# Performance work log

Measured on AMD Instinct MI355X. Metric: run time of the kernel, lower is better.

Reference implementation:

```python
import jax, jax.numpy as jnp
import numpy as np

B, L, D, E, H = 4, 2048, 512, 8, 1024

def setup_inputs() -> dict:
    key = jax.random.key(0)
    k1, k2, k3, k4 = jax.random.split(key, 4)
    x = jax.random.normal(k1, (B, L, D), dtype=jnp.float32)
    weights = jax.random.uniform(k2, (B, L, E), dtype=jnp.float32)
    w1 = jax.random.normal(k3, (E, D, H), dtype=jnp.float32) * 0.02
    b1 = jnp.zeros((E, H), dtype=jnp.float32)
    w2 = jax.random.normal(k4, (E, H, D), dtype=jnp.float32) * 0.02
    b2 = jnp.zeros((E, D), dtype=jnp.float32)
    return {"x": x, "weights": weights, "w1": w1, "b1": b1, "w2": w2, "b2": b2}

def reference(x, weights, w1, b1, w2, b2):
    # h: [B, L, E, H]
    h = jnp.einsum('bld,edh->bleh', x, w1) + b1[None, None, :, :]
    h = jax.nn.gelu(h, approximate=False)  # torch F.gelu default is exact (erf)
    # out: [B, L, E, D]
    out = jnp.einsum('bleh,ehd->bled', h, w2) + b2[None, None, :, :]
    # weighted sum over experts -> [B, L, D]
    return jnp.einsum('bled,ble->bld', out, weights)
```

## Files before the change

### kernel.cpp

```cpp
#include <hip/hip_runtime.h>
#include <hip/hip_bf16.h>

#define DEV __device__ __forceinline__

typedef __bf16 bf16;
typedef __bf16 bf16x4 __attribute__((ext_vector_type(4)));
typedef __bf16 bf16x8 __attribute__((ext_vector_type(8)));
typedef float f32x4 __attribute__((ext_vector_type(4)));

static constexpr int Bb = 4, Ll = 2048, Dd = 512, Ee = 8, Hh = 1024;
static constexpr int Mm = Bb * Ll;
static constexpr int GKS = Ee * Hh;

DEV void gload_lds16(const void* g, void* l) {
  __builtin_amdgcn_global_load_lds(
      (const __attribute__((address_space(1))) unsigned int*)g,
      (__attribute__((address_space(3))) unsigned int*)l, 16, 0, 0);
}

DEV float gelu_fast(float h) {
  const float k = 0.7978845608028654f * 2.0f * 1.4426950408889634f;
  float h2 = h * h;
  float y = h * (k + (0.044715f * k) * h2);
  float t = exp2f(y);
  return h - h * __frcp_rn(t + 1.0f);
}

__global__ void cvt_x_kernel(const float* __restrict__ in, bf16* __restrict__ out, int n4) {
  int i = blockIdx.x * blockDim.x + threadIdx.x;
  if (i < n4) {
    float4 v = ((const float4*)in)[i];
    bf16x4 o = {(bf16)v.x, (bf16)v.y, (bf16)v.z, (bf16)v.w};
    ((bf16x4*)out)[i] = o;
  }
}

__global__ void transpose_cvt(const float* __restrict__ in, bf16* __restrict__ out,
                              int R, int C, size_t in_es, size_t out_es, int out_rs) {
  __shared__ float tile[64][65];
  const int e = blockIdx.z;
  const float* ip = in + (size_t)e * in_es;
  bf16* op = out + (size_t)e * out_es;
  const int r0 = blockIdx.y * 64, c0 = blockIdx.x * 64;
  const int tc = threadIdx.x & 63, tr = threadIdx.x >> 6;
#pragma unroll
  for (int i = 0; i < 16; ++i) {
    const int r = tr + i * 4;
    tile[r][tc] = ip[(size_t)(r0 + r) * C + c0 + tc];
  }
  __syncthreads();
  const int wr = threadIdx.x & 63, wc0 = threadIdx.x >> 6;
#pragma unroll
  for (int i = 0; i < 16; ++i) {
    const int c = wc0 + i * 4;
    op[(size_t)(c0 + c) * out_rs + r0 + wr] = (bf16)tile[wr][c];
  }
}

template <int ARS, int BRS>
DEV void gemm_core(const bf16* __restrict__ Ag, const bf16* __restrict__ Bg,
                   int ksteps, f32x4 (&acc)[4][4], bf16* As, bf16* Bs) {
  const int t = threadIdx.x;
  const int lane = t & 63;
  const int w = t >> 6;
  const int srow = t >> 3;
  const int sseg = t & 7;
  const int wr = w >> 1, wc = w & 1;
  const int fr = lane & 15;
  const int fg = lane >> 4;

  for (int s = 0; s < ksteps; ++s) {
    __syncthreads();
#pragma unroll
    for (int i = 0; i < 4; ++i) {
      const int row = i * 32 + srow;
      const int q = sseg ^ (row & 7);
      gload_lds16(Ag + (size_t)row * ARS + s * 64 + q * 8,
                  (char*)As + i * 4096 + w * 1024);
      gload_lds16(Bg + (size_t)row * BRS + s * 64 + q * 8,
                  (char*)Bs + i * 4096 + w * 1024);
    }
    __syncthreads();
#pragma unroll
    for (int kk = 0; kk < 2; ++kk) {
      bf16x8 af[4], bfr[4];
#pragma unroll
      for (int mi = 0; mi < 4; ++mi) {
        const int row = wr * 64 + mi * 16 + fr;
        const int q = (kk * 4 + fg) ^ (row & 7);
        af[mi] = *(const bf16x8*)((const char*)As + row * 128 + q * 16);
      }
#pragma unroll
      for (int ni = 0; ni < 4; ++ni) {
        const int row = wc * 64 + ni * 16 + fr;
        const int q = (kk * 4 + fg) ^ (row & 7);
        bfr[ni] = *(const bf16x8*)((const char*)Bs + row * 128 + q * 16);
      }
#pragma unroll
      for (int mi = 0; mi < 4; ++mi)
#pragma unroll
        for (int ni = 0; ni < 4; ++ni)
          acc[mi][ni] = __builtin_amdgcn_mfma_f32_16x16x32_bf16(
              af[mi], bfr[ni], acc[mi][ni], 0, 0, 0);
    }
  }
}

DEV void gemm_core_r(const bf16* __restrict__ Ag, size_t a_rs,
                     const bf16* __restrict__ Bg, size_t b_rs,
                     int ksteps, f32x4 (&acc)[4][4], bf16* As, bf16* Bs) {
  const int t = threadIdx.x;
  const int lane = t & 63;
  const int w = t >> 6;
  const int srow = t >> 3;
  const int sseg = t & 7;
  const int wr = w >> 1, wc = w & 1;
  const int fr = lane & 15;
  const int fg = lane >> 4;
  for (int s = 0; s < ksteps; ++s) {
    __syncthreads();
#pragma unroll
    for (int i = 0; i < 4; ++i) {
      const int row = i * 32 + srow;
      const int q = sseg ^ (row & 7);
      gload_lds16(Ag + (size_t)row * a_rs + s * 64 + q * 8,
                  (char*)As + i * 4096 + w * 1024);
      gload_lds16(Bg + (size_t)row * b_rs + s * 64 + q * 8,
                  (char*)Bs + i * 4096 + w * 1024);
    }
    __syncthreads();
#pragma unroll
    for (int kk = 0; kk < 2; ++kk) {
      bf16x8 af[4], bfr[4];
#pragma unroll
      for (int mi = 0; mi < 4; ++mi) {
        const int row = wr * 64 + mi * 16 + fr;
        const int q = (kk * 4 + fg) ^ (row & 7);
        af[mi] = *(const bf16x8*)((const char*)As + row * 128 + q * 16);
      }
#pragma unroll
      for (int ni = 0; ni < 4; ++ni) {
        const int row = wc * 64 + ni * 16 + fr;
        const int q = (kk * 4 + fg) ^ (row & 7);
        bfr[ni] = *(const bf16x8*)((const char*)Bs + row * 128 + q * 16);
      }
#pragma unroll
      for (int mi = 0; mi < 4; ++mi)
#pragma unroll
        for (int ni = 0; ni < 4; ++ni)
          acc[mi][ni] = __builtin_amdgcn_mfma_f32_16x16x32_bf16(
              af[mi], bfr[ni], acc[mi][ni], 0, 0, 0);
    }
  }
}

__global__ __launch_bounds__(256) void ffn_stage1_t(
    const bf16* __restrict__ xb, const bf16* __restrict__ w1t,
    const float* __restrict__ b1, const float* __restrict__ wts,
    bf16* __restrict__ G) {
  __shared__ __align__(16) bf16 As[128 * 64];
  __shared__ __align__(16) bf16 Bs[128 * 64];
  __shared__ float b1s[128];
  __shared__ float wls[128];
  const int mt = blockIdx.x, ht = blockIdx.y, e = blockIdx.z;
  const int t = threadIdx.x;
  if (t < 128) b1s[t] = b1[e * Hh + ht * 128 + t];
  else wls[t - 128] = wts[((size_t)mt * 128 + (t - 128)) * Ee + e];

  f32x4 acc[4][4] = {};
  const bf16* Ag = xb + (size_t)mt * 128 * Dd;
  const bf16* Bg = w1t + ((size_t)e * Hh + (size_t)ht * 128) * Dd;
  gemm_core<Dd, Dd>(Ag, Bg, Dd / 64, acc, As, Bs);

  const int lane = t & 63, w = t >> 6;
  const int wr = w >> 1, wc = w & 1, fr = lane & 15, fq = lane >> 4;
  float bcol[4];
#pragma unroll
  for (int ni = 0; ni < 4; ++ni) bcol[ni] = b1s[wc * 64 + ni * 16 + fr];
  bf16* gp = G + ((size_t)mt * 128 + wr * 64 + fq * 4) * GKS
               + (size_t)e * Hh + ht * 128 + wc * 64 + fr;
#pragma unroll
  for (int mi = 0; mi < 4; ++mi) {
#pragma unroll
    for (int r = 0; r < 4; ++r) {
      const float wgt = wls[wr * 64 + mi * 16 + fq * 4 + r];
#pragma unroll
      for (int ni = 0; ni < 4; ++ni) {
        float v = acc[mi][ni][r] + bcol[ni];
        gp[(size_t)(mi * 16 + r) * GKS + ni * 16] = (bf16)(gelu_fast(v) * wgt);
      }
    }
  }
}

__global__ __launch_bounds__(256) void ffn_stage2_partial(
    const bf16* __restrict__ G, const bf16* __restrict__ w2t,
    float* __restrict__ P, int kchunk) {
  __shared__ __align__(16) bf16 As[128 * 64];
  __shared__ __align__(16) bf16 Bs[128 * 64];
  const int mt = blockIdx.x, nt = blockIdx.y, s = blockIdx.z;
  f32x4 acc[4][4] = {};
  const bf16* Ag = G + (size_t)mt * 128 * GKS + (size_t)s * kchunk;
  const bf16* Bg = w2t + (size_t)nt * 128 * GKS + (size_t)s * kchunk;
  gemm_core<GKS, GKS>(Ag, Bg, kchunk / 64, acc, As, Bs);

  float* Pp = P + (size_t)s * Mm * Dd;
  const int t = threadIdx.x;
  const int lane = t & 63, w = t >> 6;
  const int wr = w >> 1, wc = w & 1, fr = lane & 15, fq = lane >> 4;
#pragma unroll
  for (int mi = 0; mi < 4; ++mi)
#pragma unroll
    for (int r = 0; r < 4; ++r) {
      const size_t m = (size_t)mt * 128 + wr * 64 + mi * 16 + fq * 4 + r;
#pragma unroll
      for (int ni = 0; ni < 4; ++ni) {
        const int d = nt * 128 + wc * 64 + ni * 16 + fr;
        Pp[m * Dd + d] = acc[mi][ni][r];
      }
    }
}

__global__ __launch_bounds__(256) void reduce_bias(
    const float* __restrict__ P, const float* __restrict__ wts,
    const float* __restrict__ b2, float* __restrict__ out, int S) {
  const int n4 = Mm * Dd / 4;
  int i = blockIdx.x * 256 + threadIdx.x;
  if (i >= n4) return;
  const int m = i / (Dd / 4);
  const int d0 = (i % (Dd / 4)) * 4;
  float4 a = ((const float4*)P)[i];
  for (int s = 1; s < S; ++s) {
    float4 p = ((const float4*)P)[(size_t)s * n4 + i];
    a.x += p.x; a.y += p.y; a.z += p.z; a.w += p.w;
  }
  const float* wr = wts + (size_t)m * Ee;
#pragma unroll
  for (int e = 0; e < Ee; ++e) {
    const float w = wr[e];
    float4 b = *(const float4*)(b2 + e * Dd + d0);
    a.x += w * b.x; a.y += w * b.y; a.z += w * b.z; a.w += w * b.w;
  }
  ((float4*)out)[i] = a;
}

__global__ __launch_bounds__(256) void ffn_stage1(
    const bf16* __restrict__ xb, const bf16* __restrict__ w1t,
    const float* __restrict__ b1, const float* __restrict__ wts,
    bf16* __restrict__ G, int e0, int gks) {
  __shared__ __align__(16) bf16 As[128 * 64];
  __shared__ __align__(16) bf16 Bs[128 * 64];
  const int mt = blockIdx.x, ht = blockIdx.y, le = blockIdx.z;
  const int e = e0 + le;
  f32x4 acc[4][4] = {};
  const bf16* Ag = xb + (size_t)mt * 128 * Dd;
  const bf16* Bg = w1t + ((size_t)e * Hh + (size_t)ht * 128) * Dd;
  gemm_core_r(Ag, Dd, Bg, Dd, Dd / 64, acc, As, Bs);
  const int t = threadIdx.x;
  const int lane = t & 63, w = t >> 6;
  const int wr = w >> 1, wc = w & 1, fr = lane & 15, fq = lane >> 4;
#pragma unroll
  for (int mi = 0; mi < 4; ++mi)
#pragma unroll
    for (int r = 0; r < 4; ++r) {
      const int m = mt * 128 + wr * 64 + mi * 16 + fq * 4 + r;
      const float wgt = wts[(size_t)m * Ee + e];
#pragma unroll
      for (int ni = 0; ni < 4; ++ni) {
        const int h = ht * 128 + wc * 64 + ni * 16 + fr;
        float v = acc[mi][ni][r] + b1[e * Hh + h];
        G[(size_t)m * gks + (size_t)le * Hh + h] = (bf16)(gelu_fast(v) * wgt);
      }
    }
}

__global__ __launch_bounds__(256) void ffn_stage2(
    const bf16* __restrict__ G, const bf16* __restrict__ w2t,
    const float* __restrict__ b2, const float* __restrict__ wts,
    float* __restrict__ out, int e0, int gks, int first) {
  __shared__ __align__(16) bf16 As[128 * 64];
  __shared__ __align__(16) bf16 Bs[128 * 64];
  __shared__ float b2s[Ee][128];
  __shared__ float wls[128][Ee];
  const int mt = blockIdx.x, nt = blockIdx.y;
  const int t = threadIdx.x;
  if (first) {
    for (int i = t; i < Ee * 128; i += 256) {
      const int ee = i >> 7, d = i & 127;
      b2s[ee][d] = b2[ee * Dd + nt * 128 + d];
    }
    for (int i = t; i < 128 * Ee; i += 256) {
      const int r = i >> 3, ee = i & 7;
      wls[r][ee] = wts[((size_t)mt * 128 + r) * Ee + ee];
    }
  }
  f32x4 acc[4][4] = {};
  const bf16* Ag = G + (size_t)mt * 128 * gks;
  const bf16* Bg = w2t + (size_t)nt * 128 * ((size_t)Ee * Hh) + (size_t)e0 * Hh;
  gemm_core_r(Ag, gks, Bg, (size_t)Ee * Hh, gks / 64, acc, As, Bs);
  const int lane = t & 63, w = t >> 6;
  const int wr = w >> 1, wc = w & 1, fr = lane & 15, fq = lane >> 4;
#pragma unroll
  for (int mi = 0; mi < 4; ++mi)
#pragma unroll
    for (int r = 0; r < 4; ++r) {
      const int lrow = wr * 64 + mi * 16 + fq * 4 + r;
      const size_t m = (size_t)mt * 128 + lrow;
#pragma unroll
      for (int ni = 0; ni < 4; ++ni) {
        const int lcol = wc * 64 + ni * 16 + fr;
        const size_t oidx = m * Dd + nt * 128 + lcol;
        float v = acc[mi][ni][r];
        if (first) {
          float bias = 0.f;
#pragma unroll
          for (int ee = 0; ee < Ee; ++ee) bias += wls[lrow][ee] * b2s[ee][lcol];
          out[oidx] = v + bias;
        } else {
          out[oidx] += v;
        }
      }
    }
}

extern "C" void kernel_launch(void* const* d_in, const int* in_sizes, int n_in,
                              void* d_out, int out_size, void* d_ws, size_t ws_size,
                              hipStream_t stream) {
  const float* x   = (const float*)d_in[0];
  const float* wts = (const float*)d_in[1];
  const float* w1  = (const float*)d_in[2];
  const float* b1  = (const float*)d_in[3];
  const float* w2  = (const float*)d_in[4];
  const float* b2  = (const float*)d_in[5];
  float* out = (float*)d_out;

  char* ws = (char*)d_ws;
  size_t off = 0;
  bf16* xb  = (bf16*)(ws + off); off += (size_t)Mm * Dd * 2;
  bf16* w1t = (bf16*)(ws + off); off += (size_t)Ee * Hh * Dd * 2;
  bf16* w2t = (bf16*)(ws + off); off += (size_t)Dd * Ee * Hh * 2;

  const size_t gfull = (size_t)Mm * Ee * Hh * 2;
  const size_t psz   = (size_t)Mm * Dd * 4;

  cvt_x_kernel<<<(Mm * Dd / 4 + 255) / 256, 256, 0, stream>>>(x, xb, Mm * Dd / 4);
  transpose_cvt<<<dim3(Hh / 64, Dd / 64, Ee), 256, 0, stream>>>(
      w1, w1t, Dd, Hh, (size_t)Dd * Hh, (size_t)Hh * Dd, Dd);
  transpose_cvt<<<dim3(Dd / 64, Hh / 64, Ee), 256, 0, stream>>>(
      w2, w2t, Hh, Dd, (size_t)Hh * Dd, (size_t)Hh, Ee * Hh);

  int S = 0;
  if (ws_size >= off + gfull + 4 * psz) S = 4;
  else if (ws_size >= off + gfull + 2 * psz) S = 2;

  if (S >= 2) {
    bf16* G = (bf16*)(ws + off);
    float* P = (float*)(ws + off + gfull);
    ffn_stage1_t<<<dim3(Mm / 128, Hh / 128, Ee), 256, 0, stream>>>(
        xb, w1t, b1, wts, G);
    ffn_stage2_partial<<<dim3(Mm / 128, Dd / 128, S), 256, 0, stream>>>(
        G, w2t, P, GKS / S);
    reduce_bias<<<(Mm * Dd / 4 + 255) / 256, 256, 0, stream>>>(P, wts, b2, out, S);
  } else {
    bf16* G = (bf16*)(ws + off);
    size_t avail = ws_size > off ? ws_size - off : 0;
    size_t slab = (size_t)Mm * Hh * 2;
    int Ec = (int)(avail / slab);
    if (Ec < 1) Ec = 1;
    if (Ec > Ee) Ec = Ee;
    int first = 1;
    for (int e0 = 0; e0 < Ee;) {
      const int ec = (Ee - e0 < Ec) ? (Ee - e0) : Ec;
      const int gks = ec * Hh;
      ffn_stage1<<<dim3(Mm / 128, Hh / 128, ec), 256, 0, stream>>>(
          xb, w1t, b1, wts, G, e0, gks);
      ffn_stage2<<<dim3(Mm / 128, Dd / 128), 256, 0, stream>>>(
          G, w2t, b2, wts, out, e0, gks, first);
      e0 += ec;
      first = 0;
    }
  }
}
```

Measured before the change: 240.0 us.

## Use 256x256 double-buffered MFMA tiles for both FFN GEMM stages

Adds a 512-thread GEMM core that computes 256x256 output tiles. It double-buffers the global-to-LDS loads behind vmcnt waits and raises wave priority around the MFMA bursts. Both stage kernels switch to this core and store their epilogues as vector writes (bf16x4 / f32x4), using a transposed accumulator layout. The larger tiles are meant to improve operand reuse and hide load latency. The cost is 128KB of LDS per block, which limits occupancy, and the low-workspace expert-chunked fallback path is removed.

```diff
diff --git a/kernel.cpp b/kernel.cpp
--- a/kernel.cpp
+++ b/kernel.cpp
@@ -58,167 +58,146 @@
 }
 
 template <int ARS, int BRS>
-DEV void gemm_core(const bf16* __restrict__ Ag, const bf16* __restrict__ Bg,
-                   int ksteps, f32x4 (&acc)[4][4], bf16* As, bf16* Bs) {
+DEV void gemm256_core(const bf16* __restrict__ Ag, const bf16* __restrict__ Bg,
+                      int nt, f32x4 (&acc)[8][4], char* lds) {
   const int t = threadIdx.x;
   const int lane = t & 63;
-  const int w = t >> 6;
+  const int wid = t >> 6;
+  const int wm = wid >> 2, wn = wid & 3;
+  const int fr = lane & 15, fg = lane >> 4;
   const int srow = t >> 3;
   const int sseg = t & 7;
-  const int wr = w >> 1, wc = w & 1;
-  const int fr = lane & 15;
-  const int fg = lane >> 4;
-
-  for (int s = 0; s < ksteps; ++s) {
-    __syncthreads();
+
+  auto stage = [&](int kt, int p) {
+    char* As = lds + p * 65536;
+    char* Bs = lds + p * 65536 + 32768;
 #pragma unroll
     for (int i = 0; i < 4; ++i) {
-      const int row = i * 32 + srow;
+      const int row = i * 64 + srow;
       const int q = sseg ^ (row & 7);
-      gload_lds16(Ag + (size_t)row * ARS + s * 64 + q * 8,
-                  (char*)As + i * 4096 + w * 1024);
-      gload_lds16(Bg + (size_t)row * BRS + s * 64 + q * 8,
-                  (char*)Bs + i * 4096 + w * 1024);
-    }
-    __syncthreads();
-#pragma unroll
-    for (int kk = 0; kk < 2; ++kk) {
-      bf16x8 af[4], bfr[4];
-#pragma unroll
-      for (int mi = 0; mi < 4; ++mi) {
-        const int row = wr * 64 + mi * 16 + fr;
-        const int q = (kk * 4 + fg) ^ (row & 7);
-        af[mi] = *(const bf16x8*)((const char*)As + row * 128 + q * 16);
-      }
-#pragma unroll
-      for (int ni = 0; ni < 4; ++ni) {
-        const int row = wc * 64 + ni * 16 + fr;
-        const int q = (kk * 4 + fg) ^ (row & 7);
-        bfr[ni] = *(const bf16x8*)((const char*)Bs + row * 128 + q * 16);
-      }
-#pragma unroll
-      for (int mi = 0; mi < 4; ++mi)
-#pragma unroll
-        for (int ni = 0; ni < 4; ++ni)
-          acc[mi][ni] = __builtin_amdgcn_mfma_f32_16x16x32_bf16(
-              af[mi], bfr[ni], acc[mi][ni], 0, 0, 0);
-    }
-  }
-}
-
-DEV void gemm_core_r(const bf16* __restrict__ Ag, size_t a_rs,
-                     const bf16* __restrict__ Bg, size_t b_rs,
-                     int ksteps, f32x4 (&acc)[4][4], bf16* As, bf16* Bs) {
-  const int t = threadIdx.x;
-  const int lane = t & 63;
-  const int w = t >> 6;
-  const int srow = t >> 3;
-  const int sseg = t & 7;
-  const int wr = w >> 1, wc = w & 1;
-  const int fr = lane & 15;
-  const int fg = lane >> 4;
-  for (int s = 0; s < ksteps; ++s) {
-    __syncthreads();
-#pragma unroll
-    for (int i = 0; i < 4; ++i) {
-      const int row = i * 32 + srow;
-      const int q = sseg ^ (row & 7);
-      gload_lds16(Ag + (size_t)row * a_rs + s * 64 + q * 8,
-                  (char*)As + i * 4096 + w * 1024);
-      gload_lds16(Bg + (size_t)row * b_rs + s * 64 + q * 8,
-                  (char*)Bs + i * 4096 + w * 1024);
-    }
-    __syncthreads();
-#pragma unroll
-    for (int kk = 0; kk < 2; ++kk) {
-      bf16x8 af[4], bfr[4];
-#pragma unroll
-      for (int mi = 0; mi < 4; ++mi) {
-        const int row = wr * 64 + mi * 16 + fr;
-        const int q = (kk * 4 + fg) ^ (row & 7);
-        af[mi] = *(const bf16x8*)((const char*)As + row * 128 + q * 16);
-      }
-#pragma unroll
-      for (int ni = 0; ni < 4; ++ni) {
-        const int row = wc * 64 + ni * 16 + fr;
-        const int q = (kk * 4 + fg) ^ (row & 7);
-        bfr[ni] = *(const bf16x8*)((const char*)Bs + row * 128 + q * 16);
-      }
-#pragma unroll
-      for (int mi = 0; mi < 4; ++mi)
-#pragma unroll
-        for (int ni = 0; ni < 4; ++ni)
-          acc[mi][ni] = __builtin_amdgcn_mfma_f32_16x16x32_bf16(
-              af[mi], bfr[ni], acc[mi][ni], 0, 0, 0);
-    }
-  }
-}
-
-__global__ __launch_bounds__(256) void ffn_stage1_t(
+      gload_lds16(Ag + (size_t)row * ARS + kt * 64 + q * 8, As + i * 8192 + wid * 1024);
+      gload_lds16(Bg + (size_t)row * BRS + kt * 64 + q * 8, Bs + i * 8192 + wid * 1024);
+    }
+  };
+
+  stage(0, 0);
+  for (int kt = 0; kt < nt; ++kt) {
+    const int p = kt & 1;
+    if (kt + 1 < nt) {
+      stage(kt + 1, p ^ 1);
+      asm volatile("s_waitcnt vmcnt(8)" ::: "memory");
+    } else {
+      asm volatile("s_waitcnt vmcnt(0)" ::: "memory");
+    }
+    __builtin_amdgcn_s_barrier();
+    const char* As = lds + p * 65536;
+    const char* Bs = lds + p * 65536 + 32768;
+    bf16x8 bfrag[4][2];
+#pragma unroll
+    for (int q = 0; q < 4; ++q) {
+      if (q == 0) {
+#pragma unroll
+        for (int fj = 0; fj < 4; ++fj)
+#pragma unroll
+          for (int kk = 0; kk < 2; ++kk) {
+            const int row = wn * 64 + fj * 16 + fr;
+            const int seg = (kk * 4 + fg) ^ (row & 7);
+            bfrag[fj][kk] = *(const bf16x8*)(Bs + row * 128 + seg * 16);
+          }
+      }
+      bf16x8 af[2][2];
+#pragma unroll
+      for (int fil = 0; fil < 2; ++fil)
+#pragma unroll
+        for (int kk = 0; kk < 2; ++kk) {
+          const int row = wm * 128 + (q * 2 + fil) * 16 + fr;
+          const int seg = (kk * 4 + fg) ^ (row & 7);
+          af[fil][kk] = *(const bf16x8*)(As + row * 128 + seg * 16);
+        }
+      __builtin_amdgcn_s_barrier();
+      asm volatile("s_waitcnt lgkmcnt(0)" ::: "memory");
+      __builtin_amdgcn_sched_barrier(0);
+      __builtin_amdgcn_s_setprio(1);
+#pragma unroll
+      for (int fil = 0; fil < 2; ++fil)
+#pragma unroll
+        for (int fj = 0; fj < 4; ++fj)
+#pragma unroll
+          for (int kk = 0; kk < 2; ++kk)
+            acc[q * 2 + fil][fj] = __builtin_amdgcn_mfma_f32_16x16x32_bf16(
+                bfrag[fj][kk], af[fil][kk], acc[q * 2 + fil][fj], 0, 0, 0);
+      __builtin_amdgcn_s_setprio(0);
+      __builtin_amdgcn_s_barrier();
+    }
+  }
+}
+
+__global__ __launch_bounds__(512, 2) void ffn_stage1_256(
     const bf16* __restrict__ xb, const bf16* __restrict__ w1t,
     const float* __restrict__ b1, const float* __restrict__ wts,
     bf16* __restrict__ G) {
-  __shared__ __align__(16) bf16 As[128 * 64];
-  __shared__ __align__(16) bf16 Bs[128 * 64];
-  __shared__ float b1s[128];
-  __shared__ float wls[128];
-  const int mt = blockIdx.x, ht = blockIdx.y, e = blockIdx.z;
-  const int t = threadIdx.x;
-  if (t < 128) b1s[t] = b1[e * Hh + ht * 128 + t];
-  else wls[t - 128] = wts[((size_t)mt * 128 + (t - 128)) * Ee + e];
-
-  f32x4 acc[4][4] = {};
-  const bf16* Ag = xb + (size_t)mt * 128 * Dd;
-  const bf16* Bg = w1t + ((size_t)e * Hh + (size_t)ht * 128) * Dd;
-  gemm_core<Dd, Dd>(Ag, Bg, Dd / 64, acc, As, Bs);
-
-  const int lane = t & 63, w = t >> 6;
-  const int wr = w >> 1, wc = w & 1, fr = lane & 15, fq = lane >> 4;
-  float bcol[4];
-#pragma unroll
-  for (int ni = 0; ni < 4; ++ni) bcol[ni] = b1s[wc * 64 + ni * 16 + fr];
-  bf16* gp = G + ((size_t)mt * 128 + wr * 64 + fq * 4) * GKS
-               + (size_t)e * Hh + ht * 128 + wc * 64 + fr;
-#pragma unroll
-  for (int mi = 0; mi < 4; ++mi) {
-#pragma unroll
-    for (int r = 0; r < 4; ++r) {
-      const float wgt = wls[wr * 64 + mi * 16 + fq * 4 + r];
-#pragma unroll
-      for (int ni = 0; ni < 4; ++ni) {
-        float v = acc[mi][ni][r] + bcol[ni];
-        gp[(size_t)(mi * 16 + r) * GKS + ni * 16] = (bf16)(gelu_fast(v) * wgt);
-      }
-    }
-  }
-}
-
-__global__ __launch_bounds__(256) void ffn_stage2_partial(
+  __shared__ __align__(16) char lds[131072];
+  __shared__ float b1s[256];
+  __shared__ float wls[256];
+  const int mt = blockIdx.x;
+  const int e = blockIdx.y >> 2, ht2 = blockIdx.y & 3;
+  const int t = threadIdx.x;
+  if (t < 256) b1s[t] = b1[e * Hh + ht2 * 256 + t];
+  else wls[t - 256] = wts[((size_t)mt * 256 + (t - 256)) * Ee + e];
+
+  f32x4 acc[8][4] = {};
+  const bf16* Ag = xb + (size_t)mt * 256 * Dd;
+  const bf16* Bg = w1t + ((size_t)e * Hh + (size_t)ht2 * 256) * Dd;
+  gemm256_core<Dd, Dd>(Ag, Bg, Dd / 64, acc, lds);
+
+  const int lane = t & 63, wid = t >> 6;
+  const int wm = wid >> 2, wn = wid & 3;
+  const int fr = lane & 15, fq = lane >> 4;
+  float b1v[4][4];
+#pragma unroll
+  for (int fj = 0; fj < 4; ++fj)
+#pragma unroll
+    for (int r = 0; r < 4; ++r) b1v[fj][r] = b1s[wn * 64 + fj * 16 + fq * 4 + r];
+#pragma unroll
+  for (int fi = 0; fi < 8; ++fi) {
+    const int m = mt * 256 + wm * 128 + fi * 16 + fr;
+    const float wgt = wls[wm * 128 + fi * 16 + fr];
+    bf16* gp = G + (size_t)m * GKS + e * Hh + ht2 * 256 + wn * 64 + fq * 4;
+#pragma unroll
+    for (int fj = 0; fj < 4; ++fj) {
+      bf16x4 o;
+#pragma unroll
+      for (int r = 0; r < 4; ++r) {
+        float v = acc[fi][fj][r] + b1v[fj][r];
+        o[r] = (bf16)(gelu_fast(v) * wgt);
+      }
+      *(bf16x4*)(gp + fj * 16) = o;
+    }
+  }
+}
+
+__global__ __launch_bounds__(512, 2) void ffn_stage2_256(
     const bf16* __restrict__ G, const bf16* __restrict__ w2t,
     float* __restrict__ P, int kchunk) {
-  __shared__ __align__(16) bf16 As[128 * 64];
-  __shared__ __align__(16) bf16 Bs[128 * 64];
+  __shared__ __align__(16) char lds[131072];
   const int mt = blockIdx.x, nt = blockIdx.y, s = blockIdx.z;
-  f32x4 acc[4][4] = {};
-  const bf16* Ag = G + (size_t)mt * 128 * GKS + (size_t)s * kchunk;
-  const bf16* Bg = w2t + (size_t)nt * 128 * GKS + (size_t)s * kchunk;
-  gemm_core<GKS, GKS>(Ag, Bg, kchunk / 64, acc, As, Bs);
+  f32x4 acc[8][4] = {};
+  const bf16* Ag = G + (size_t)mt * 256 * GKS + (size_t)s * kchunk;
+  const bf16* Bg = w2t + (size_t)nt * 256 * GKS + (size_t)s * kchunk;
+  gemm256_core<GKS, GKS>(Ag, Bg, kchunk / 64, acc, lds);
 
   float* Pp = P + (size_t)s * Mm * Dd;
   const int t = threadIdx.x;
-  const int lane = t & 63, w = t >> 6;
-  const int wr = w >> 1, wc = w & 1, fr = lane & 15, fq = lane >> 4;
-#pragma unroll
-  for (int mi = 0; mi < 4; ++mi)
-#pragma unroll
-    for (int r = 0; r < 4; ++r) {
-      const size_t m = (size_t)mt * 128 + wr * 64 + mi * 16 + fq * 4 + r;
-#pragma unroll
-      for (int ni = 0; ni < 4; ++ni) {
-        const int d = nt * 128 + wc * 64 + ni * 16 + fr;
-        Pp[m * Dd + d] = acc[mi][ni][r];
-      }
-    }
+  const int lane = t & 63, wid = t >> 6;
+  const int wm = wid >> 2, wn = wid & 3;
+  const int fr = lane & 15, fq = lane >> 4;
+#pragma unroll
+  for (int fi = 0; fi < 8; ++fi) {
+    const size_t m = (size_t)mt * 256 + wm * 128 + fi * 16 + fr;
+    float* pp = Pp + m * Dd + nt * 256 + wn * 64 + fq * 4;
+#pragma unroll
+    for (int fj = 0; fj < 4; ++fj) *(f32x4*)(pp + fj * 16) = acc[fi][fj];
+  }
 }
 
 __global__ __launch_bounds__(256) void reduce_bias(
@@ -244,81 +223,113 @@
   ((float4*)out)[i] = a;
 }
 
-__global__ __launch_bounds__(256) void ffn_stage1(
+template <int ARS, int BRS>
+DEV void gemm_core(const bf16* __restrict__ Ag, const bf16* __restrict__ Bg,
+                   int ksteps, f32x4 (&acc)[4][4], bf16* As, bf16* Bs) {
+  const int t = threadIdx.x;
+  const int lane = t & 63;
+  const int w = t >> 6;
+  const int srow = t >> 3;
+  const int sseg = t & 7;
+  const int wr = w >> 1, wc = w & 1;
+  const int fr = lane & 15;
+  const int fg = lane >> 4;
+  for (int s = 0; s < ksteps; ++s) {
+    __syncthreads();
+#pragma unroll
+    for (int i = 0; i < 4; ++i) {
+      const int row = i * 32 + srow;
+      const int q = sseg ^ (row & 7);
+      gload_lds16(Ag + (size_t)row * ARS + s * 64 + q * 8,
+                  (char*)As + i * 4096 + w * 1024);
+      gload_lds16(Bg + (size_t)row * BRS + s * 64 + q * 8,
+                  (char*)Bs + i * 4096 + w * 1024);
+    }
+    __syncthreads();
+#pragma unroll
+    for (int kk = 0; kk < 2; ++kk) {
+      bf16x8 af[4], bfr[4];
+#pragma unroll
+      for (int mi = 0; mi < 4; ++mi) {
+        const int row = wr * 64 + mi * 16 + fr;
+        const int q = (kk * 4 + fg) ^ (row & 7);
+        af[mi] = *(const bf16x8*)((const char*)As + row * 128 + q * 16);
+      }
+#pragma unroll
+      for (int ni = 0; ni < 4; ++ni) {
+        const int row = wc * 64 + ni * 16 + fr;
+        const int q = (kk * 4 + fg) ^ (row & 7);
+        bfr[ni] = *(const bf16x8*)((const char*)Bs + row * 128 + q * 16);
+      }
+#pragma unroll
+      for (int mi = 0; mi < 4; ++mi)
+#pragma unroll
+        for (int ni = 0; ni < 4; ++ni)
+          acc[mi][ni] = __builtin_amdgcn_mfma_f32_16x16x32_bf16(
+              af[mi], bfr[ni], acc[mi][ni], 0, 0, 0);
+    }
+  }
+}
+
+__global__ __launch_bounds__(256) void ffn_stage1_t(
     const bf16* __restrict__ xb, const bf16* __restrict__ w1t,
     const float* __restrict__ b1, const float* __restrict__ wts,
-    bf16* __restrict__ G, int e0, int gks) {
+    bf16* __restrict__ G) {
   __shared__ __align__(16) bf16 As[128 * 64];
   __shared__ __align__(16) bf16 Bs[128 * 64];
-  const int mt = blockIdx.x, ht = blockIdx.y, le = blockIdx.z;
-  const int e = e0 + le;
+  __shared__ float b1s[128];
+  __shared__ float wls[128];
+  const int mt = blockIdx.x, ht = blockIdx.y, e = blockIdx.z;
+  const int t = threadIdx.x;
+  if (t < 128) b1s[t] = b1[e * Hh + ht * 128 + t];
+  else wls[t - 128] = wts[((size_t)mt * 128 + (t - 128)) * Ee + e];
   f32x4 acc[4][4] = {};
   const bf16* Ag = xb + (size_t)mt * 128 * Dd;
   const bf16* Bg = w1t + ((size_t)e * Hh + (size_t)ht * 128) * Dd;
-  gemm_core_r(Ag, Dd, Bg, Dd, Dd / 64, acc, As, Bs);
-  const int t = threadIdx.x;
+  gemm_core<Dd, Dd>(Ag, Bg, Dd / 64, acc, As, Bs);
   const int lane = t & 63, w = t >> 6;
   const int wr = w >> 1, wc = w & 1, fr = lane & 15, fq = lane >> 4;
+  float bcol[4];
+#pragma unroll
+  for (int ni = 0; ni < 4; ++ni) bcol[ni] = b1s[wc * 64 + ni * 16 + fr];
+  bf16* gp = G + ((size_t)mt * 128 + wr * 64 + fq * 4) * GKS
+               + (size_t)e * Hh + ht * 128 + wc * 64 + fr;
 #pragma unroll
   for (int mi = 0; mi < 4; ++mi)
 #pragma unroll
     for (int r = 0; r < 4; ++r) {
-      const int m = mt * 128 + wr * 64 + mi * 16 + fq * 4 + r;
-      const float wgt = wts[(size_t)m * Ee + e];
+      const float wgt = wls[wr * 64 + mi * 16 + fq * 4 + r];
 #pragma unroll
       for (int ni = 0; ni < 4; ++ni) {
-        const int h = ht * 128 + wc * 64 + ni * 16 + fr;
-        float v = acc[mi][ni][r] + b1[e * Hh + h];
-        G[(size_t)m * gks + (size_t)le * Hh + h] = (bf16)(gelu_fast(v) * wgt);
-      }
-    }
-}
-
-__global__ __launch_bounds__(256) void ffn_stage2(
+        float v = acc[mi][ni][r] + bcol[ni];
+        gp[(size_t)(mi * 16 + r) * GKS + ni * 16] = (bf16)(gelu_fast(v) * wgt);
+      }
+    }
+}
+
+__global__ __launch_bounds__(256) void ffn_stage2_partial(
     const bf16* __restrict__ G, const bf16* __restrict__ w2t,
-    const float* __restrict__ b2, const float* __restrict__ wts,
-    float* __restrict__ out, int e0, int gks, int first) {
+    float* __restrict__ P, int kchunk) {
   __shared__ __align__(16) bf16 As[128 * 64];
   __shared__ __align__(16) bf16 Bs[128 * 64];
-  __shared__ float b2s[Ee][128];
-  __shared__ float wls[128][Ee];
-  const int mt = blockIdx.x, nt = blockIdx.y;
-  const int t = threadIdx.x;
-  if (first) {
-    for (int i = t; i < Ee * 128; i += 256) {
-      const int ee = i >> 7, d = i & 127;
-      b2s[ee][d] = b2[ee * Dd + nt * 128 + d];
-    }
-    for (int i = t; i < 128 * Ee; i += 256) {
-      const int r = i >> 3, ee = i & 7;
-      wls[r][ee] = wts[((size_t)mt * 128 + r) * Ee + ee];
-    }
-  }
+  const int mt = blockIdx.x, nt = blockIdx.y, s = blockIdx.z;
   f32x4 acc[4][4] = {};
-  const bf16* Ag = G + (size_t)mt * 128 * gks;
-  const bf16* Bg = w2t + (size_t)nt * 128 * ((size_t)Ee * Hh) + (size_t)e0 * Hh;
-  gemm_core_r(Ag, gks, Bg, (size_t)Ee * Hh, gks / 64, acc, As, Bs);
+  const bf16* Ag = G + (size_t)mt * 128 * GKS + (size_t)s * kchunk;
+  const bf16* Bg = w2t + (size_t)nt * 128 * GKS + (size_t)s * kchunk;
+  gemm_core<GKS, GKS>(Ag, Bg, kchunk / 64, acc, As, Bs);
+  float* Pp = P + (size_t)s * Mm * Dd;
+  const int t = threadIdx.x;
   const int lane = t & 63, w = t >> 6;
   const int wr = w >> 1, wc = w & 1, fr = lane & 15, fq = lane >> 4;
 #pragma unroll
   for (int mi = 0; mi < 4; ++mi)
 #pragma unroll
     for (int r = 0; r < 4; ++r) {
-      const int lrow = wr * 64 + mi * 16 + fq * 4 + r;
-      const size_t m = (size_t)mt * 128 + lrow;
+      const size_t m = (size_t)mt * 128 + wr * 64 + mi * 16 + fq * 4 + r;
 #pragma unroll
       for (int ni = 0; ni < 4; ++ni) {
-        const int lcol = wc * 64 + ni * 16 + fr;
-        const size_t oidx = m * Dd + nt * 128 + lcol;
-        float v = acc[mi][ni][r];
-        if (first) {
-          float bias = 0.f;
-#pragma unroll
-          for (int ee = 0; ee < Ee; ++ee) bias += wls[lrow][ee] * b2s[ee][lcol];
-          out[oidx] = v + bias;
-        } else {
-          out[oidx] += v;
-        }
+        const int d = nt * 128 + wc * 64 + ni * 16 + fr;
+        Pp[m * Dd + d] = acc[mi][ni][r];
       }
     }
 }
@@ -349,35 +360,21 @@
   transpose_cvt<<<dim3(Dd / 64, Hh / 64, Ee), 256, 0, stream>>>(
       w2, w2t, Hh, Dd, (size_t)Hh * Dd, (size_t)Hh, Ee * Hh);
 
-  int S = 0;
-  if (ws_size >= off + gfull + 4 * psz) S = 4;
-  else if (ws_size >= off + gfull + 2 * psz) S = 2;
-
-  if (S >= 2) {
+  if (ws_size >= off + gfull + 4 * psz) {
+    bf16* G = (bf16*)(ws + off);
+    float* P = (float*)(ws + off + gfull);
+    ffn_stage1_256<<<dim3(Mm / 256, (Ee * Hh) / 256), 512, 0, stream>>>(
+        xb, w1t, b1, wts, G);
+    ffn_stage2_256<<<dim3(Mm / 256, Dd / 256, 4), 512, 0, stream>>>(
+        G, w2t, P, GKS / 4);
+    reduce_bias<<<(Mm * Dd / 4 + 255) / 256, 256, 0, stream>>>(P, wts, b2, out, 4);
+  } else if (ws_size >= off + gfull + 2 * psz) {
     bf16* G = (bf16*)(ws + off);
     float* P = (float*)(ws + off + gfull);
     ffn_stage1_t<<<dim3(Mm / 128, Hh / 128, Ee), 256, 0, stream>>>(
         xb, w1t, b1, wts, G);
-    ffn_stage2_partial<<<dim3(Mm / 128, Dd / 128, S), 256, 0, stream>>>(
-        G, w2t, P, GKS / S);
-    reduce_bias<<<(Mm * Dd / 4 + 255) / 256, 256, 0, stream>>>(P, wts, b2, out, S);
-  } else {
-    bf16* G = (bf16*)(ws + off);
-    size_t avail = ws_size > off ? ws_size - off : 0;
-    size_t slab = (size_t)Mm * Hh * 2;
-    int Ec = (int)(avail / slab);
-    if (Ec < 1) Ec = 1;
-    if (Ec > Ee) Ec = Ee;
-    int first = 1;
-    for (int e0 = 0; e0 < Ee;) {
-      const int ec = (Ee - e0 < Ec) ? (Ee - e0) : Ec;
-      const int gks = ec * Hh;
-      ffn_stage1<<<dim3(Mm / 128, Hh / 128, ec), 256, 0, stream>>>(
-          xb, w1t, b1, wts, G, e0, gks);
-      ffn_stage2<<<dim3(Mm / 128, Dd / 128), 256, 0, stream>>>(
-          G, w2t, b2, wts, out, e0, gks, first);
-      e0 += ec;
-      first = 0;
-    }
-  }
-}
+    ffn_stage2_partial<<<dim3(Mm / 128, Dd / 128, 2), 256, 0, stream>>>(
+        G, w2t, P, GKS / 2);
+    reduce_bias<<<(Mm * Dd / 4 + 255) / 256, 256, 0, stream>>>(P, wts, b2, out, 2);
+  }
+}
```

Measured after the change: 220.9 us. -8.0%, faster.
